# Kernel optimization log

Measured on AMD Instinct MI355X. Metric: run time of the kernel, lower is better.

Reference implementation:

```python
import jax, jax.numpy as jnp
import numpy as np
import math

NUM_HEADS = 16
HEAVY_RATIO = 0.1
RECENT_RATIO = 0.1
ROPE_THETA = 10000.0


def setup_inputs() -> dict:
    key = jax.random.key(0)
    ks = jax.random.split(key, 5)
    b, s, h = 1, 2048, 2048
    return {
        "hidden_states": jax.random.normal(ks[0], (b, s, h), dtype=jnp.float32),
        "Wq": jax.random.normal(ks[1], (h, h), dtype=jnp.float32) * 0.02,
        "Wk": jax.random.normal(ks[2], (h, h), dtype=jnp.float32) * 0.02,
        "Wv": jax.random.normal(ks[3], (h, h), dtype=jnp.float32) * 0.02,
        "Wo": jax.random.normal(ks[4], (h, h), dtype=jnp.float32) * 0.02,
    }


def _rotate_half(x):
    d = x.shape[-1]
    return jnp.concatenate([-x[..., d // 2:], x[..., : d // 2]], axis=-1)


def _rope(q, k, seq_len, head_dim, dtype):
    # LLaMA rotary embedding: inv_freq over even dims, emb = [freqs, freqs]
    inv_freq = 1.0 / (ROPE_THETA ** (jnp.arange(0, head_dim, 2, dtype=jnp.float32) / head_dim))
    pos = jnp.arange(seq_len, dtype=jnp.float32)
    freqs = pos[:, None] * inv_freq[None, :]            # [s, d/2]
    emb = jnp.concatenate([freqs, freqs], axis=-1)       # [s, d]
    cos = jnp.cos(emb).astype(dtype)[None, None]         # [1,1,s,d]
    sin = jnp.sin(emb).astype(dtype)[None, None]
    q = q * cos + _rotate_half(q) * sin
    k = k * cos + _rotate_half(k) * sin
    return q, k


def reference(hidden_states, Wq, Wk, Wv, Wo):
    b, s, hidden = hidden_states.shape
    H = NUM_HEADS
    d = hidden // H

    def proj(W):  # nn.Linear(x) = x @ W.T, then split heads -> [b,H,s,d]
        return (hidden_states @ W.T).reshape(b, s, H, d).transpose(0, 2, 1, 3)

    q, k, v = proj(Wq), proj(Wk), proj(Wv)
    q, k = _rope(q, k, s, d, hidden_states.dtype)

    scores = jnp.einsum("bhqd,bhkd->bhqk", q, k) / math.sqrt(d)  # [b,H,s,s]
    neg = jnp.finfo(scores.dtype).min
    i = jnp.arange(s)[:, None]
    j = jnp.arange(s)[None, :]
    causal = jnp.where(j <= i, jnp.array(0.0, scores.dtype), neg)
    scores = jnp.maximum(scores + causal, neg)

    heavy_budget = int(HEAVY_RATIO * s)
    recent_budget = int(RECENT_RATIO * s)

    # first softmax (fp32), accumulate column importances
    tmp_attn = jax.nn.softmax(scores.astype(jnp.float32), axis=-1).astype(scores.dtype)
    tmp_sum = jnp.sum(tmp_attn, axis=-2)                 # [b,H,s]
    _, topk_idx = jax.lax.top_k(tmp_sum, heavy_budget)   # [b,H,heavy]
    heavy_mask = jnp.any(topk_idx[..., :, None] == jnp.arange(s)[None, None, None, :], axis=-2)  # [b,H,s]

    # recent band: tril(diag=recent) & triu(diag=-recent)  <=>  |i-j| <= recent
    band = jnp.abs(i - j) <= recent_budget               # [s,s]
    mask = heavy_mask[:, :, None, :] | band[None, None]

    scores = jnp.where(mask, scores, neg)
    probs = jax.nn.softmax(scores.astype(jnp.float32), axis=-1).astype(q.dtype)
    attn = jnp.einsum("bhqk,bhkd->bhqd", probs, v)
    attn = attn.transpose(0, 2, 1, 3).reshape(b, s, hidden)
    return attn @ Wo.T
```

## Files before the change

kernel.cpp:

```cpp
#include <hip/hip_runtime.h>
#include <hip/hip_bf16.h>
#include <stdint.h>

#define SEQ   2048
#define HIDN  2048
#define NHEAD 16
#define HDIM  128
#define HEAVY 204
#define RECENT 204

typedef __attribute__((ext_vector_type(4))) float f32x4;
typedef __attribute__((ext_vector_type(8))) short bf16x8;
typedef unsigned short u16;
typedef unsigned int   u32;

static __device__ __forceinline__ u16 f2bf(float f){
  union { float f; u32 u; } v; v.f = f;
  u32 r = (v.u + 0x7FFFu + ((v.u >> 16) & 1u)) >> 16;
  return (u16)r;
}
static __device__ __forceinline__ float bf2f(u16 u){
  union { u32 u; float f; } v; v.u = ((u32)u) << 16;
  return v.f;
}

static __device__ __forceinline__ void gload16(const void* g, void* l){
  __builtin_amdgcn_global_load_lds((const __attribute__((address_space(1))) u32*)g,
                                   (__attribute__((address_space(3))) u32*)l, 16, 0, 0);
}

#define WAITVM(N) asm volatile("s_waitcnt vmcnt(" #N ")" ::: "memory")
#define LGKM0RAW  asm volatile("s_waitcnt lgkmcnt(0)" ::: "memory")
#define BARRAW    __builtin_amdgcn_s_barrier()
#define PRIO1     __builtin_amdgcn_s_setprio(1)
#define PRIO0     __builtin_amdgcn_s_setprio(0)

static __device__ __forceinline__ void stage_tile(const u16* __restrict__ base, size_t stride,
                                                  int row0, u16* __restrict__ lds, int tid){
  const int wbase = tid & ~63;
#pragma unroll
  for (int it = 0; it < 4; ++it){
    int m = it * 256 + tid;
    int row = m >> 4, cp = m & 15;
    gload16(base + (size_t)(row0 + row) * stride + ((cp ^ (row & 7)) * 8),
            lds + (it * 256 + wbase) * 8);
  }
}

static __device__ __forceinline__ void stage64_512(const u16* __restrict__ base, int row0,
                                                   u16* __restrict__ lds, int tid){
#pragma unroll
  for (int it = 0; it < 2; ++it){
    int m = it * 512 + tid;
    int row = m >> 4, cp = m & 15;
    gload16(base + (size_t)(row0 + row) * 2048 + ((cp ^ (row & 7)) * 8),
            lds + (it * 512 + (tid & ~63)) * 8);
  }
}
static __device__ __forceinline__ void stage128_512(const u16* __restrict__ base, int row0,
                                                    u16* __restrict__ lds, int tid){
#pragma unroll
  for (int it = 0; it < 4; ++it){
    int m = it * 512 + tid;
    int row = m >> 4, cp = m & 15;
    gload16(base + (size_t)(row0 + row) * 2048 + ((cp ^ (row & 7)) * 8),
            lds + (it * 512 + (tid & ~63)) * 8);
  }
}

__global__ void k_cvt5(const float* __restrict__ A0, const float* __restrict__ A1,
                       const float* __restrict__ A2, const float* __restrict__ A3,
                       const float* __restrict__ A4, u16* __restrict__ out){
  int id = blockIdx.x * 256 + threadIdx.x;
  int sel = id >> 20, off = (id & 1048575) * 4;
  const float* src = sel == 0 ? A0 : sel == 1 ? A1 : sel == 2 ? A2 : sel == 3 ? A3 : A4;
  float4 v = *(const float4*)(src + off);
  ushort4 o;
  o.x = f2bf(v.x); o.y = f2bf(v.y); o.z = f2bf(v.z); o.w = f2bf(v.w);
  *(ushort4*)(out + (size_t)sel * 4194304 + off) = o;
}

__global__ void k_rope_tab(float* __restrict__ cosT, float* __restrict__ sinT){
  int i = blockIdx.x * 256 + threadIdx.x;
  int pos = i >> 6, j = i & 63;
  float invf = powf(10000.0f, -(float)j * (1.0f / 64.0f));
  float a = (float)pos * invf;
  cosT[i] = cosf(a);
  sinT[i] = sinf(a);
}

__global__ void k_rope2(u16* __restrict__ Qm, u16* __restrict__ Km,
                        const float* __restrict__ cosT, const float* __restrict__ sinT){
  int gid = blockIdx.x * 256 + threadIdx.x;
  u16* M = (gid < 524288) ? Qm : Km;
  int id = gid & 524287;
  int pos = id >> 8, rem = id & 255;
  int h = rem >> 4, j4 = (rem & 15) * 4;
  u16* p = M + (size_t)pos * HIDN + h * HDIM + j4;
  ushort4 lo = *(ushort4*)p;
  ushort4 hi = *(ushort4*)(p + 64);
  float4 c = *(const float4*)(cosT + pos * 64 + j4);
  float4 s = *(const float4*)(sinT + pos * 64 + j4);
  float l0 = bf2f(lo.x), l1 = bf2f(lo.y), l2 = bf2f(lo.z), l3 = bf2f(lo.w);
  float h0 = bf2f(hi.x), h1 = bf2f(hi.y), h2 = bf2f(hi.z), h3 = bf2f(hi.w);
  ushort4 nlo, nhi;
  nlo.x = f2bf(l0 * c.x - h0 * s.x);  nhi.x = f2bf(h0 * c.x + l0 * s.x);
  nlo.y = f2bf(l1 * c.y - h1 * s.y);  nhi.y = f2bf(h1 * c.y + l1 * s.y);
  nlo.z = f2bf(l2 * c.z - h2 * s.z);  nhi.z = f2bf(h2 * c.z + l2 * s.z);
  nlo.w = f2bf(l3 * c.w - h3 * s.w);  nhi.w = f2bf(h3 * c.w + l3 * s.w);
  *(ushort4*)p = nlo;
  *(ushort4*)(p + 64) = nhi;
}

__global__ void k_zero4(float* __restrict__ p, int n4){
  for (int i = blockIdx.x * 256 + threadIdx.x; i < n4; i += gridDim.x * 256)
    ((float4*)p)[i] = (float4){0.f, 0.f, 0.f, 0.f};
}

__global__ __launch_bounds__(512, 1)
void k_g256(const u16* __restrict__ X, const u16* __restrict__ Wq, const u16* __restrict__ Wk,
            const u16* __restrict__ Wv, u16* __restrict__ C0, u16* __restrict__ C1,
            u16* __restrict__ C2){
  __shared__ __align__(16) u16 LA[2][256 * 64];
  __shared__ __align__(16) u16 LB[2][192 * 64];
  const int tid = threadIdx.x;
  const int lane = tid & 63, wvi = tid >> 6;
  const int wm = wvi >> 2, wn = wvi & 3;
  const int g = lane >> 4, c15 = lane & 15;
  const int brow = blockIdx.y * 256;
  const int bcol = blockIdx.x * 192;
  const int NT = 32;

  f32x4 acc[8][3];
#pragma unroll
  for (int m = 0; m < 8; m++)
#pragma unroll
    for (int n = 0; n < 3; n++) acc[m][n] = (f32x4){0.f, 0.f, 0.f, 0.f};

  const int cc0 = ((g ^ (c15 & 7)) * 8);
  bf16x8 af[4][2], bf[3][2];

#define BPTR(rB_) (rB_ < 2048 ? Wq + (size_t)(rB_) * 2048 \
                 : rB_ < 4096 ? Wk + (size_t)((rB_) - 2048) * 2048 \
                              : Wv + (size_t)((rB_) - 4096) * 2048)
#define STGA(grow0, gcol0, ldsb) do { \
  _Pragma("unroll") for (int it = 0; it < 2; ++it){ \
    int m_ = it * 512 + tid; \
    int row_ = m_ >> 3, cp_ = m_ & 7; \
    gload16(X + (size_t)((grow0) + row_) * 2048 + (gcol0) + ((cp_ ^ (row_ & 7)) * 8), \
            (ldsb) + (it * 512 + (tid & ~63)) * 8); \
  } } while(0)
#define STGB128(gcol0, ldsb) do { \
  _Pragma("unroll") for (int it = 0; it < 2; ++it){ \
    int m_ = it * 512 + tid; \
    int row_ = m_ >> 3, cp_ = m_ & 7; \
    int rB_ = bcol + row_; \
    const u16* bp_ = BPTR(rB_); \
    gload16(bp_ + (gcol0) + ((cp_ ^ (row_ & 7)) * 8), \
            (ldsb) + (it * 512 + (tid & ~63)) * 8); \
  } } while(0)
#define STGB64(gcol0, ldsb) do { \
    int row_ = 128 + (tid >> 3), cp_ = tid & 7; \
    int rB_ = bcol + row_; \
    const u16* bp_ = BPTR(rB_); \
    gload16(bp_ + (gcol0) + ((cp_ ^ (row_ & 7)) * 8), \
            (ldsb) + (tid & ~63) * 8); \
  } while(0)
#define RDA(buf, mibase) \
  _Pragma("unroll") for (int mi2 = 0; mi2 < 4; ++mi2){ \
    const u16* pr = &LA[buf][0] + (size_t)(wm * 128 + ((mibase) + mi2) * 16 + c15) * 64; \
    af[mi2][0] = *(const bf16x8*)(pr + cc0); \
    af[mi2][1] = *(const bf16x8*)(pr + (cc0 ^ 32)); \
  }
#define RDB2(buf) \
  _Pragma("unroll") for (int ni2 = 0; ni2 < 2; ++ni2){ \
    const u16* pr = &LB[buf][0] + (size_t)(wn * 48 + ni2 * 16 + c15) * 64; \
    bf[ni2][0] = *(const bf16x8*)(pr + cc0); \
    bf[ni2][1] = *(const bf16x8*)(pr + (cc0 ^ 32)); \
  }
#define RDB1(buf) do { \
    const u16* pr = &LB[buf][0] + (size_t)(wn * 48 + 32 + c15) * 64; \
    bf[2][0] = *(const bf16x8*)(pr + cc0); \
    bf[2][1] = *(const bf16x8*)(pr + (cc0 ^ 32)); \
  } while(0)
#define MM2(mibase) \
  _Pragma("unroll") for (int mi2 = 0; mi2 < 4; ++mi2) \
  _Pragma("unroll") for (int ni2 = 0; ni2 < 2; ++ni2) \
  _Pragma("unroll") for (int kk = 0; kk < 2; ++kk) \
    acc[(mibase) + mi2][ni2] = __builtin_amdgcn_mfma_f32_16x16x32_bf16( \
        af[mi2][kk], bf[ni2][kk], acc[(mibase) + mi2][ni2], 0, 0, 0);
#define MM1(mibase) \
  _Pragma("unroll") for (int mi2 = 0; mi2 < 4; ++mi2) \
  _Pragma("unroll") for (int kk = 0; kk < 2; ++kk) \
    acc[(mibase) + mi2][2] = __builtin_amdgcn_mfma_f32_16x16x32_bf16( \
        af[mi2][kk], bf[2][kk], acc[(mibase) + mi2][2], 0, 0, 0);

  STGA(brow,       0, &LA[0][0]);
  STGA(brow + 128, 0, &LA[0][0] + 128 * 64);
  STGB128(0,  &LB[0][0]);
  STGB64(0,   &LB[0][0] + 128 * 64);
  STGB128(64, &LB[1][0]);
  STGB64(64,  &LB[1][0] + 128 * 64);
  WAITVM(3);
  BARRAW;

  for (int t = 0; t < NT; t += 2){
    const int kn1 = (t + 1) * 64;
    const int kn2 = (t + 2) * 64;
    const int kn3 = (t + 3) * 64;
    RDA(0, 0); RDB2(0);
    STGA(brow, kn1, &LA[1][0]);
    BARRAW; PRIO1; MM2(0); PRIO0; BARRAW;
    RDB1(0);
    STGA(brow + 128, kn1, &LA[1][0] + 128 * 64);
    BARRAW; PRIO1; MM1(0); PRIO0; BARRAW;
    RDA(0, 4);
    if (t + 2 < NT) STGB128(kn2, &LB[0][0]);
    BARRAW; PRIO1; MM1(4); PRIO0; BARRAW;
    if (t + 2 < NT){ STGB64(kn2, &LB[0][0] + 128 * 64); WAITVM(3); }
    else            { WAITVM(0); }
    BARRAW; PRIO1; MM2(4); PRIO0; BARRAW;
    RDA(1, 0); RDB2(1);
    if (t + 2 < NT) STGA(brow, kn2, &LA[0][0]);
    BARRAW; PRIO1; MM2(0); PRIO0; BARRAW;
    RDB1(1);
    if (t + 2 < NT) STGA(brow + 128, kn2, &LA[0][0] + 128 * 64);
    BARRAW; PRIO1; MM1(0); PRIO0; BARRAW;
    RDA(1, 4);
    if (t + 3 < NT) STGB128(kn3, &LB[1][0]);
    BARRAW; PRIO1; MM1(4); PRIO0; BARRAW;
    if (t + 3 < NT){ STGB64(kn3, &LB[1][0] + 128 * 64); WAITVM(3); }
    else if (t + 2 < NT){ WAITVM(0); }
    BARRAW; PRIO1; MM2(4); PRIO0; BARRAW;
  }
#undef BPTR
#undef STGA
#undef STGB128
#undef STGB64
#undef RDA
#undef RDB2
#undef RDB1
#undef MM2
#undef MM1

#pragma unroll
  for (int mi = 0; mi < 8; ++mi)
#pragma unroll
    for (int ni = 0; ni < 3; ++ni){
      int colbase = bcol + wn * 48 + ni * 16;
      int proj = colbase >> 11;
      u16* Cb = proj == 0 ? C0 : proj == 1 ? C1 : C2;
      int lc = (colbase & 2047) + c15;
#pragma unroll
      for (int r = 0; r < 4; ++r){
        int row = brow + wm * 128 + mi * 16 + g * 4 + r;
        Cb[(size_t)row * 2048 + lc] = f2bf(acc[mi][ni][r]);
      }
    }
}

static __device__ __forceinline__ void stage_g(const u16* __restrict__ A, const u16* __restrict__ B,
                                               int brow, int bcol, int k0,
                                               u16* __restrict__ as, u16* __restrict__ bs, int tid){
  const int wbase = tid & ~63;
#pragma unroll
  for (int it = 0; it < 2; ++it){
    int m = it * 256 + tid;
    int row = m >> 2, q = m & 3;
    gload16(A + (size_t)(brow + row) * 2048 + k0 + q * 8, as + (it * 256 + wbase) * 8);
    gload16(B + (size_t)(bcol + row) * 2048 + k0 + q * 8, bs + (it * 256 + wbase) * 8);
  }
}

__global__ __launch_bounds__(256)
void k_gemm_out(const u16* __restrict__ A, const u16* __restrict__ B, float* __restrict__ C){
  __shared__ __align__(16) u16 As[2][128 * 32];
  __shared__ __align__(16) u16 Bs[2][128 * 32];
  const int tid = threadIdx.x;
  const int w = tid >> 6, lane = tid & 63;
  const int wr = w >> 1, wc = w & 1;
  const int g = lane >> 4, c15 = lane & 15;
  const int brow = blockIdx.y * 128, bcol = blockIdx.x * 128;

  f32x4 acc[4][4];
#pragma unroll
  for (int m = 0; m < 4; m++)
#pragma unroll
    for (int n = 0; n < 4; n++) acc[m][n] = (f32x4){0.f, 0.f, 0.f, 0.f};

  stage_g(A, B, brow, bcol, 0, As[0], Bs[0], tid);
  int cur = 0;
  for (int kt = 0; kt < 64; ++kt){
    if (kt + 1 < 64){ stage_g(A, B, brow, bcol, (kt + 1) * 32, As[cur ^ 1], Bs[cur ^ 1], tid);
                      WAITVM(4); }
    else            { WAITVM(0); }
    BARRAW;
    bf16x8 af[4], bfr[4];
#pragma unroll
    for (int m = 0; m < 4; m++) af[m] = *(const bf16x8*)(As[cur] + (wr * 64 + m * 16 + c15) * 32 + g * 8);
#pragma unroll
    for (int n = 0; n < 4; n++) bfr[n] = *(const bf16x8*)(Bs[cur] + (wc * 64 + n * 16 + c15) * 32 + g * 8);
    PRIO1;
#pragma unroll
    for (int m = 0; m < 4; m++)
#pragma unroll
      for (int n = 0; n < 4; n++)
        acc[m][n] = __builtin_amdgcn_mfma_f32_16x16x32_bf16(af[m], bfr[n], acc[m][n], 0, 0, 0);
    PRIO0;
    BARRAW;
    cur ^= 1;
  }
#pragma unroll
  for (int m = 0; m < 4; m++)
#pragma unroll
    for (int n = 0; n < 4; n++)
#pragma unroll
      for (int r = 0; r < 4; r++){
        int row = brow + wr * 64 + m * 16 + g * 4 + r;
        int col = bcol + wc * 64 + n * 16 + c15;
        C[(size_t)row * 2048 + col] = acc[m][n][r];
      }
}

__global__ void k_transpose_v(const u16* __restrict__ V, u16* __restrict__ Vt){
  __shared__ u16 t[32][33];
  int s0 = blockIdx.x * 32, c0 = blockIdx.y * 32;
  int tid = threadIdx.x;
  int r = tid >> 3, cc = (tid & 7) * 4;
  ushort4 v = *(const ushort4*)(V + (size_t)(s0 + r) * 2048 + c0 + cc);
  t[r][cc] = v.x; t[r][cc + 1] = v.y; t[r][cc + 2] = v.z; t[r][cc + 3] = v.w;
  __syncthreads();
  int co = tid >> 3, ro = (tid & 7) * 4;
  ushort4 o;
  o.x = t[ro][co]; o.y = t[ro + 1][co]; o.z = t[ro + 2][co]; o.w = t[ro + 3][co];
  *(ushort4*)(Vt + (size_t)(c0 + co) * 2048 + s0 + ro) = o;
}

__global__ __launch_bounds__(512)
void k_pass1a(const u16* __restrict__ Q, const u16* __restrict__ K, float* __restrict__ rowsum){
  __shared__ __align__(16) u16 Qs[128 * 128];
  __shared__ __align__(16) u16 Ks[2][64 * 128];
  const int tid = threadIdx.x;
  const int wv = tid >> 6, lane = tid & 63;
  const int g = lane >> 4, c15 = lane & 15;
  const int h = blockIdx.y;
  int qb = 0, c = 0;
  { int rem = blockIdx.x; int q = 0;
    while (rem >= ((2 * q + 9) >> 3)){ rem -= (2 * q + 9) >> 3; q++; }
    qb = q; c = rem; }
  const int i0 = qb * 128;
  const int ktend = 2 * qb + 2;
  const int kt0 = c * 8;
  const int kt1 = (ktend < kt0 + 8) ? ktend : (kt0 + 8);
  const u16* Qh = Q + h * HDIM;
  const u16* Kh = K + h * HDIM;
  const float scale = 0.08838834764831845f;
  const int arow = wv * 16 + c15;

  stage128_512(Qh, i0, Qs, tid);
  stage64_512(Kh, kt0 * 64, Ks[0], tid);

  float lsum[4] = {0.f, 0.f, 0.f, 0.f};
  int cur = 0;
  for (int kt = kt0; kt < kt1; ++kt){
    if (kt + 1 < kt1){ stage64_512(Kh, (kt + 1) * 64, Ks[cur ^ 1], tid); WAITVM(2); }
    else             { WAITVM(0); }
    BARRAW;
    const int k0 = kt * 64;
    f32x4 sacc[4];
#pragma unroll
    for (int n = 0; n < 4; n++) sacc[n] = (f32x4){0.f, 0.f, 0.f, 0.f};
#pragma unroll
    for (int ks = 0; ks < 4; ++ks){
      bf16x8 a = *(const bf16x8*)(Qs + arow * 128 + ((ks * 32 + g * 8) ^ ((arow & 7) << 3)));
#pragma unroll
      for (int n = 0; n < 4; n++){
        int brw = n * 16 + c15;
        bf16x8 b = *(const bf16x8*)(Ks[cur] + brw * 128 + ((ks * 32 + g * 8) ^ ((brw & 7) << 3)));
        sacc[n] = __builtin_amdgcn_mfma_f32_16x16x32_bf16(a, b, sacc[n], 0, 0, 0);
      }
    }
    if (kt < 2 * qb){
#pragma unroll
      for (int n = 0; n < 4; n++)
#pragma unroll
        for (int r = 0; r < 4; r++)
          lsum[r] += __expf(sacc[n][r] * scale);
    } else {
#pragma unroll
      for (int n = 0; n < 4; n++){
        int col = k0 + n * 16 + c15;
#pragma unroll
        for (int r = 0; r < 4; r++){
          int rowg = i0 + wv * 16 + g * 4 + r;
          lsum[r] += (col <= rowg) ? __expf(sacc[n][r] * scale) : 0.f;
        }
      }
    }
    BARRAW;
    cur ^= 1;
  }
#pragma unroll
  for (int r = 0; r < 4; r++){
    float v = lsum[r];
    v += __shfl_xor(v, 1); v += __shfl_xor(v, 2);
    v += __shfl_xor(v, 4); v += __shfl_xor(v, 8);
    lsum[r] = v;
  }
  if (c15 == 0){
#pragma unroll
    for (int r = 0; r < 4; r++)
      atomicAdd(&rowsum[h * 2048 + i0 + wv * 16 + g * 4 + r], lsum[r]);
  }
}

__global__ __launch_bounds__(512)
void k_pass1b(const u16* __restrict__ Q, const u16* __restrict__ K,
              const float* __restrict__ rowsum, float* __restrict__ colsum){
  __shared__ __align__(16) u16 Ks[128 * 128];
  __shared__ __align__(16) u16 Qs[2][64 * 128];
  __shared__ float rsb[512];
  const int tid = threadIdx.x;
  const int wv = tid >> 6, lane = tid & 63;
  const int g = lane >> 4, c15 = lane & 15;
  const int h = blockIdx.y;
  int kb = 0, c = 0;
  { int rem = blockIdx.x; int q = 0;
    while (rem >= ((39 - 2 * q) >> 3)){ rem -= (39 - 2 * q) >> 3; q++; }
    kb = q; c = rem; }
  const int k0 = kb * 128;
  const int qt0 = 2 * kb + c * 8;
  const int qt1 = (2 * kb + c * 8 + 8 < 32) ? (2 * kb + c * 8 + 8) : 32;
  const u16* Qh = Q + h * HDIM;
  const u16* Kh = K + h * HDIM;
  const float scale = 0.08838834764831845f;
  const int bcol = wv * 16 + c15;

  { int row = qt0 * 64 + tid;
    float rv = (row < 2048) ? rowsum[h * 2048 + row] : 1.0f;
    rsb[tid] = 1.0f / rv; }
  stage128_512(Kh, k0, Ks, tid);
  stage64_512(Qh, qt0 * 64, Qs[0], tid);
  LGKM0RAW;

  float racc = 0.f;
  int cur = 0;
  for (int qt = qt0; qt < qt1; ++qt){
    if (qt + 1 < qt1){ stage64_512(Qh, (qt + 1) * 64, Qs[cur ^ 1], tid); WAITVM(2); }
    else             { WAITVM(0); }
    BARRAW;
    const int i0q = qt * 64;
    f32x4 sacc[4];
#pragma unroll
    for (int m = 0; m < 4; m++) sacc[m] = (f32x4){0.f, 0.f, 0.f, 0.f};
#pragma unroll
    for (int ks = 0; ks < 4; ++ks){
      bf16x8 b = *(const bf16x8*)(Ks + bcol * 128 + ((ks * 32 + g * 8) ^ ((bcol & 7) << 3)));
#pragma unroll
      for (int m = 0; m < 4; m++){
        int arw = m * 16 + c15;
        bf16x8 a = *(const bf16x8*)(Qs[cur] + arw * 128 + ((ks * 32 + g * 8) ^ ((arw & 7) << 3)));
        sacc[m] = __builtin_amdgcn_mfma_f32_16x16x32_bf16(a, b, sacc[m], 0, 0, 0);
      }
    }
    const int rbase = (qt - qt0) * 64;
    if (qt >= 2 * kb + 2){
#pragma unroll
      for (int m = 0; m < 4; m++)
#pragma unroll
        for (int r = 0; r < 4; r++){
          int rl = m * 16 + g * 4 + r;
          racc += __expf(sacc[m][r] * scale) * rsb[rbase + rl];
        }
    } else {
      const int col = k0 + bcol;
#pragma unroll
      for (int m = 0; m < 4; m++)
#pragma unroll
        for (int r = 0; r < 4; r++){
          int rl = m * 16 + g * 4 + r;
          int rowg = i0q + rl;
          racc += (col <= rowg) ? __expf(sacc[m][r] * scale) * rsb[rbase + rl] : 0.f;
        }
    }
    BARRAW;
    cur ^= 1;
  }
  racc += __shfl_xor(racc, 16);
  racc += __shfl_xor(racc, 32);
  if (g == 0) atomicAdd(&colsum[h * 2048 + k0 + bcol], racc);
}

__global__ __launch_bounds__(1024)
void k_topk(const float* __restrict__ colsum, short* __restrict__ cidx){
  __shared__ float v[2048];
  __shared__ short ix[2048];
  __shared__ short sx[256];
  const int tid = threadIdx.x;
  const int h = blockIdx.x;
  for (int i = tid; i < 2048; i += 1024){ v[i] = colsum[h * 2048 + i]; ix[i] = (short)i; }
  __syncthreads();
  for (int k = 2; k <= 2048; k <<= 1){
    for (int j = k >> 1; j > 0; j >>= 1){
      int i = ((tid / j) * (j << 1)) + (tid % j);
      int l = i + j;
      float vi = v[i], vl = v[l];
      short ii = ix[i], il = ix[l];
      bool before_i = (vi > vl) || (vi == vl && ii < il);
      bool dir = (i & k) == 0;
      if (dir ? !before_i : before_i){ v[i] = vl; v[l] = vi; ix[i] = il; ix[l] = ii; }
      __syncthreads();
    }
  }
  if (tid < 256) sx[tid] = (tid < HEAVY) ? ix[tid] : (short)32767;
  __syncthreads();
  for (int k = 2; k <= 256; k <<= 1){
    for (int j = k >> 1; j > 0; j >>= 1){
      if (tid < 128){
        int i = ((tid / j) * (j << 1)) + (tid % j);
        int l = i + j;
        short a = sx[i], b = sx[l];
        bool asc = (i & k) == 0;
        if (asc ? (a > b) : (a < b)){ sx[i] = b; sx[l] = a; }
      }
      __syncthreads();
    }
  }
  if (tid < 256) cidx[h * 256 + tid] = sx[tid];
}

__global__ void k_gatherK(const u16* __restrict__ Kb, const short* __restrict__ cidx,
                          u16* __restrict__ Kg){
  int gid = blockIdx.x * 256 + threadIdx.x;
  int h = gid >> 12, rem = gid & 4095;
  int slot = rem >> 4, cp = rem & 15;
  int cid = cidx[h * 256 + slot];
  bf16x8 z = (bf16x8){0,0,0,0,0,0,0,0};
  bf16x8 val = (cid < 2048) ? *(const bf16x8*)(Kb + (size_t)cid * 2048 + h * 128 + cp * 8) : z;
  *(bf16x8*)(Kg + ((size_t)h * 256 + slot) * 128 + cp * 8) = val;
}

__global__ void k_gatherV(const u16* __restrict__ Vb, const short* __restrict__ cidx,
                          u16* __restrict__ Vg){
  __shared__ __align__(16) u16 t[32][136];
  int h = blockIdx.x >> 3, s0 = (blockIdx.x & 7) * 32;
  int tid = threadIdx.x;
#pragma unroll
  for (int it = 0; it < 2; ++it){
    int m = it * 256 + tid;
    int s = m >> 4, cp = m & 15;
    int cid = cidx[h * 256 + s0 + s];
    bf16x8 z = (bf16x8){0,0,0,0,0,0,0,0};
    bf16x8 val = (cid < 2048) ? *(const bf16x8*)(Vb + (size_t)cid * 2048 + h * 128 + cp * 8) : z;
    *(bf16x8*)(&t[s][cp * 8]) = val;
  }
  __syncthreads();
#pragma unroll
  for (int i = 0; i < 16; ++i){
    int idx = i * 256 + tid;
    int d = idx >> 5, s = idx & 31;
    Vg[((size_t)h * 128 + d) * 256 + s0 + s] = t[s][d];
  }
}

static __device__ __forceinline__ void load_vf(const u16* __restrict__ Vt,
                                               const u16* __restrict__ Vg,
                                               int h, int e, int g, int c15,
                                               bf16x8 vf[2][8]){
  const bool isg = (e >= 100);
#pragma unroll
  for (int ks2 = 0; ks2 < 2; ++ks2)
#pragma unroll
    for (int f = 0; f < 8; ++f){
      int vrow = f * 16 + c15;
      vf[ks2][f] = isg
        ? *(const bf16x8*)(Vg + ((size_t)h * 128 + vrow) * 256 + (e - 100) * 64 + ks2 * 32 + g * 8)
        : *(const bf16x8*)(Vt + ((size_t)h * 128 + vrow) * 2048 + e * 64 + ks2 * 32 + g * 8);
    }
}

__global__ __launch_bounds__(256)
void k_pass2(const u16* __restrict__ Q, const u16* __restrict__ K, const u16* __restrict__ Vt,
             const u16* __restrict__ Kg, const u16* __restrict__ Vg,
             const short* __restrict__ cidx, u16* __restrict__ attn){
  __shared__ __align__(16) u16 Qs[64 * 128];
  __shared__ __align__(16) u16 Ks[2][64 * 128];
  __shared__ __align__(16) u16 Ps[4][16 * 64];
  __shared__ short cids[256];
  __shared__ int lists[12];
  __shared__ int nact_s;
  const int tid = threadIdx.x;
  const int w = tid >> 6, lane = tid & 63;
  const int g = lane >> 4, c15 = lane & 15;
  const int qb = blockIdx.x, h = blockIdx.y;
  const int i0 = qb * 64;
  const u16* Qh = Q + h * HDIM;
  const u16* Kh = K + h * HDIM;
  const u16* Kgh = Kg + (size_t)h * 256 * 128;
  const float scale = 0.08838834764831845f;
  const int arow = w * 16 + c15;

  if (tid < 256) cids[tid] = cidx[h * 256 + tid];
  __syncthreads();
  if (tid == 0){
    int n = 0;
    int ktb0 = (i0 > RECENT) ? ((i0 - RECENT) >> 6) : 0;
    for (int kt = ktb0; kt <= qb; ++kt) lists[n++] = kt;
    for (int gt = 0; gt < 4; ++gt)
      if ((int)cids[gt * 64] <= i0 - RECENT + 62) lists[n++] = 100 + gt;
    nact_s = n;
  }
  __syncthreads();
  const int nact = nact_s;

  stage_tile(Qh, 2048, i0, Qs, tid);
  { int e = lists[0];
    if (e < 100) stage_tile(Kh, 2048, e * 64, Ks[0], tid);
    else         stage_tile(Kgh, 128, (e - 100) * 64, Ks[0], tid); }
  bf16x8 vf[2][8];
  load_vf(Vt, Vg, h, lists[0], g, c15, vf);
  WAITVM(16);
  BARRAW;

  f32x4 oacc[8];
#pragma unroll
  for (int f = 0; f < 8; f++) oacc[f] = (f32x4){0.f, 0.f, 0.f, 0.f};
  float lsum[4] = {0.f, 0.f, 0.f, 0.f};

  int cur = 0;
  for (int i = 0; i < nact; ++i){
    const int e = lists[i];
    const bool isg = (e >= 100);
    const bool nxt = (i + 1 < nact);
    if (nxt){
      int e2 = lists[i + 1];
      if (e2 < 100) stage_tile(Kh, 2048, e2 * 64, Ks[cur ^ 1], tid);
      else          stage_tile(Kgh, 128, (e2 - 100) * 64, Ks[cur ^ 1], tid);
      WAITVM(20);
    } else {
      WAITVM(16);
    }
    BARRAW;
    f32x4 sacc[4];
#pragma unroll
    for (int n = 0; n < 4; n++) sacc[n] = (f32x4){0.f, 0.f, 0.f, 0.f};
#pragma unroll
    for (int ks = 0; ks < 4; ++ks){
      bf16x8 a = *(const bf16x8*)(Qs + arow * 128 + ((ks * 32 + g * 8) ^ ((arow & 7) << 3)));
#pragma unroll
      for (int n = 0; n < 4; n++){
        int brw = n * 16 + c15;
        bf16x8 b = *(const bf16x8*)(Ks[cur] + brw * 128 + ((ks * 32 + g * 8) ^ ((brw & 7) << 3)));
        sacc[n] = __builtin_amdgcn_mfma_f32_16x16x32_bf16(a, b, sacc[n], 0, 0, 0);
      }
    }
#pragma unroll
    for (int n = 0; n < 4; n++){
      int cid = isg ? (int)cids[(e - 100) * 64 + n * 16 + c15] : (e * 64 + n * 16 + c15);
#pragma unroll
      for (int r = 0; r < 4; r++){
        int rowg = i0 + w * 16 + g * 4 + r;
        int dist = rowg - cid;
        bool valid = (cid <= rowg) && (isg ? (dist > RECENT) : (dist <= RECENT));
        float ev = valid ? __expf(sacc[n][r] * scale) : 0.f;
        lsum[r] += ev;
        int prow = g * 4 + r;
        Ps[w][prow * 64 + ((n * 16 + c15) ^ ((prow & 7) << 3))] = f2bf(ev);
      }
    }
    if (nxt) WAITVM(4); else WAITVM(0);
    PRIO1;
#pragma unroll
    for (int ks2 = 0; ks2 < 2; ++ks2){
      bf16x8 pa = *(const bf16x8*)(&Ps[w][c15 * 64 + ((ks2 * 32 + g * 8) ^ ((c15 & 7) << 3))]);
#pragma unroll
      for (int f = 0; f < 8; ++f)
        oacc[f] = __builtin_amdgcn_mfma_f32_16x16x32_bf16(pa, vf[ks2][f], oacc[f], 0, 0, 0);
    }
    PRIO0;
    if (nxt) load_vf(Vt, Vg, h, lists[i + 1], g, c15, vf);
    BARRAW;
    cur ^= 1;
  }
  float rinv[4];
#pragma unroll
  for (int r = 0; r < 4; r++){
    float v = lsum[r];
    v += __shfl_xor(v, 1); v += __shfl_xor(v, 2);
    v += __shfl_xor(v, 4); v += __shfl_xor(v, 8);
    rinv[r] = 1.0f / v;
  }
#pragma unroll
  for (int f = 0; f < 8; f++)
#pragma unroll
    for (int r = 0; r < 4; r++){
      int rowg = i0 + w * 16 + g * 4 + r;
      attn[(size_t)rowg * 2048 + h * HDIM + f * 16 + c15] = f2bf(oacc[f][r] * rinv[r]);
    }
}

extern "C" void kernel_launch(void* const* d_in, const int* in_sizes, int n_in,
                              void* d_out, int out_size, void* d_ws, size_t ws_size,
                              hipStream_t stream){
  const float* X  = (const float*)d_in[0];
  const float* Wq = (const float*)d_in[1];
  const float* Wk = (const float*)d_in[2];
  const float* Wv = (const float*)d_in[3];
  const float* Wo = (const float*)d_in[4];

  char* w = (char*)d_ws;
  const size_t MB8 = (size_t)2048 * 2048 * 2;
  u16* Xb  = (u16*)(w);
  u16* Wqb = (u16*)(w + 1 * MB8);
  u16* Wkb = (u16*)(w + 2 * MB8);
  u16* Wvb = (u16*)(w + 3 * MB8);
  u16* Wob = (u16*)(w + 4 * MB8);
  u16* Qb  = (u16*)(w + 5 * MB8);
  u16* Kb  = (u16*)(w + 6 * MB8);
  u16* Vb  = (u16*)(w + 7 * MB8);
  u16* Vtb   = Wqb;
  u16* attnb = Xb;
  char* p = w + 8 * MB8;
  float* cosT = (float*)p;              p += 524288;
  float* sinT = (float*)p;              p += 524288;
  float* colsum = (float*)p;            p += 131072;
  float* rowsum = (float*)p;            p += 131072;
  short* cidx  = (short*)p;             p += 16 * 256 * 2;
  u16*   Kg    = (u16*)p;               p += (size_t)16 * 256 * 128 * 2;
  u16*   Vg    = (u16*)p;

  dim3 b256(256);

  k_cvt5<<<20480, b256, 0, stream>>>(X, Wq, Wk, Wv, Wo, Xb);
  k_rope_tab<<<512, b256, 0, stream>>>(cosT, sinT);
  k_zero4<<<64, b256, 0, stream>>>(colsum, 65536 / 4);

  k_g256<<<dim3(32, 8), dim3(512), 0, stream>>>(Xb, Wqb, Wkb, Wvb, Qb, Kb, Vb);
  k_rope2<<<4096, b256, 0, stream>>>(Qb, Kb, cosT, sinT);
  k_transpose_v<<<dim3(64, 64), b256, 0, stream>>>(Vb, Vtb);

  k_pass1a<<<dim3(40, 16), dim3(512), 0, stream>>>(Qb, Kb, rowsum);
  k_pass1b<<<dim3(40, 16), dim3(512), 0, stream>>>(Qb, Kb, rowsum, colsum);
  k_topk<<<16, dim3(1024), 0, stream>>>(colsum, cidx);
  k_gatherK<<<256, b256, 0, stream>>>(Kb, cidx, Kg);
  k_gatherV<<<128, b256, 0, stream>>>(Vb, cidx, Vg);
  k_pass2<<<dim3(32, 16), b256, 0, stream>>>(Qb, Kb, Vtb, Kg, Vg, cidx, attnb);

  k_gemm_out<<<dim3(16, 16), b256, 0, stream>>>(attnb, Wob, (float*)d_out);
}
```

Before: 278.9 us.

## Merge small launches into combined kernels and restructure pass1 to register-resident tiles

Several small kernels are merged into combined launches selected by block index: the convert, rope-table and zero kernels become one, rope and V transpose become one, and the K and V gathers become one. This is meant to cut per-launch overhead and tail gaps between dependent launches. Separately, pass1a and pass1b drop to 256 threads with each wave owning 32 rows. The stationary Q or K operand now sits in registers instead of LDS, which cuts LDS use and reads but raises register pressure.

```diff
diff --git a/kernel.cpp b/kernel.cpp
--- a/kernel.cpp
+++ b/kernel.cpp
@@ -30,7 +30,6 @@
 }
 
 #define WAITVM(N) asm volatile("s_waitcnt vmcnt(" #N ")" ::: "memory")
-#define LGKM0RAW  asm volatile("s_waitcnt lgkmcnt(0)" ::: "memory")
 #define BARRAW    __builtin_amdgcn_s_barrier()
 #define PRIO1     __builtin_amdgcn_s_setprio(1)
 #define PRIO0     __builtin_amdgcn_s_setprio(0)
@@ -47,74 +46,70 @@
   }
 }
 
-static __device__ __forceinline__ void stage64_512(const u16* __restrict__ base, int row0,
-                                                   u16* __restrict__ lds, int tid){
-#pragma unroll
-  for (int it = 0; it < 2; ++it){
-    int m = it * 512 + tid;
-    int row = m >> 4, cp = m & 15;
-    gload16(base + (size_t)(row0 + row) * 2048 + ((cp ^ (row & 7)) * 8),
-            lds + (it * 512 + (tid & ~63)) * 8);
-  }
-}
-static __device__ __forceinline__ void stage128_512(const u16* __restrict__ base, int row0,
-                                                    u16* __restrict__ lds, int tid){
-#pragma unroll
-  for (int it = 0; it < 4; ++it){
-    int m = it * 512 + tid;
-    int row = m >> 4, cp = m & 15;
-    gload16(base + (size_t)(row0 + row) * 2048 + ((cp ^ (row & 7)) * 8),
-            lds + (it * 512 + (tid & ~63)) * 8);
-  }
-}
-
-__global__ void k_cvt5(const float* __restrict__ A0, const float* __restrict__ A1,
+__global__ void k_prep(const float* __restrict__ A0, const float* __restrict__ A1,
                        const float* __restrict__ A2, const float* __restrict__ A3,
-                       const float* __restrict__ A4, u16* __restrict__ out){
-  int id = blockIdx.x * 256 + threadIdx.x;
-  int sel = id >> 20, off = (id & 1048575) * 4;
-  const float* src = sel == 0 ? A0 : sel == 1 ? A1 : sel == 2 ? A2 : sel == 3 ? A3 : A4;
-  float4 v = *(const float4*)(src + off);
-  ushort4 o;
-  o.x = f2bf(v.x); o.y = f2bf(v.y); o.z = f2bf(v.z); o.w = f2bf(v.w);
-  *(ushort4*)(out + (size_t)sel * 4194304 + off) = o;
-}
-
-__global__ void k_rope_tab(float* __restrict__ cosT, float* __restrict__ sinT){
-  int i = blockIdx.x * 256 + threadIdx.x;
-  int pos = i >> 6, j = i & 63;
-  float invf = powf(10000.0f, -(float)j * (1.0f / 64.0f));
-  float a = (float)pos * invf;
-  cosT[i] = cosf(a);
-  sinT[i] = sinf(a);
-}
-
-__global__ void k_rope2(u16* __restrict__ Qm, u16* __restrict__ Km,
-                        const float* __restrict__ cosT, const float* __restrict__ sinT){
-  int gid = blockIdx.x * 256 + threadIdx.x;
-  u16* M = (gid < 524288) ? Qm : Km;
-  int id = gid & 524287;
-  int pos = id >> 8, rem = id & 255;
-  int h = rem >> 4, j4 = (rem & 15) * 4;
-  u16* p = M + (size_t)pos * HIDN + h * HDIM + j4;
-  ushort4 lo = *(ushort4*)p;
-  ushort4 hi = *(ushort4*)(p + 64);
-  float4 c = *(const float4*)(cosT + pos * 64 + j4);
-  float4 s = *(const float4*)(sinT + pos * 64 + j4);
-  float l0 = bf2f(lo.x), l1 = bf2f(lo.y), l2 = bf2f(lo.z), l3 = bf2f(lo.w);
-  float h0 = bf2f(hi.x), h1 = bf2f(hi.y), h2 = bf2f(hi.z), h3 = bf2f(hi.w);
-  ushort4 nlo, nhi;
-  nlo.x = f2bf(l0 * c.x - h0 * s.x);  nhi.x = f2bf(h0 * c.x + l0 * s.x);
-  nlo.y = f2bf(l1 * c.y - h1 * s.y);  nhi.y = f2bf(h1 * c.y + l1 * s.y);
-  nlo.z = f2bf(l2 * c.z - h2 * s.z);  nhi.z = f2bf(h2 * c.z + l2 * s.z);
-  nlo.w = f2bf(l3 * c.w - h3 * s.w);  nhi.w = f2bf(h3 * c.w + l3 * s.w);
-  *(ushort4*)p = nlo;
-  *(ushort4*)(p + 64) = nhi;
-}
-
-__global__ void k_zero4(float* __restrict__ p, int n4){
-  for (int i = blockIdx.x * 256 + threadIdx.x; i < n4; i += gridDim.x * 256)
-    ((float4*)p)[i] = (float4){0.f, 0.f, 0.f, 0.f};
+                       const float* __restrict__ A4, u16* __restrict__ out,
+                       float* __restrict__ cosT, float* __restrict__ sinT,
+                       float* __restrict__ colsum){
+  int b = blockIdx.x, tid = threadIdx.x;
+  if (b < 20480){
+    int id = b * 256 + tid;
+    int sel = id >> 20, off = (id & 1048575) * 4;
+    const float* src = sel == 0 ? A0 : sel == 1 ? A1 : sel == 2 ? A2 : sel == 3 ? A3 : A4;
+    float4 v = *(const float4*)(src + off);
+    ushort4 o;
+    o.x = f2bf(v.x); o.y = f2bf(v.y); o.z = f2bf(v.z); o.w = f2bf(v.w);
+    *(ushort4*)(out + (size_t)sel * 4194304 + off) = o;
+  } else if (b < 20992){
+    int i = (b - 20480) * 256 + tid;
+    int pos = i >> 6, j = i & 63;
+    float invf = powf(10000.0f, -(float)j * (1.0f / 64.0f));
+    float a = (float)pos * invf;
+    cosT[i] = cosf(a);
+    sinT[i] = sinf(a);
+  } else {
+    int i = (b - 20992) * 256 + tid;
+    if (i < 16384) ((float4*)colsum)[i] = (float4){0.f, 0.f, 0.f, 0.f};
+  }
+}
+
+__global__ void k_post(u16* __restrict__ Qm, u16* __restrict__ Km,
+                       const float* __restrict__ cosT, const float* __restrict__ sinT,
+                       const u16* __restrict__ V, u16* __restrict__ Vt){
+  __shared__ u16 t[32][33];
+  int b = blockIdx.x, tid = threadIdx.x;
+  if (b < 4096){
+    int gid = b * 256 + tid;
+    u16* M = (gid < 524288) ? Qm : Km;
+    int id = gid & 524287;
+    int pos = id >> 8, rem = id & 255;
+    int h = rem >> 4, j4 = (rem & 15) * 4;
+    u16* p = M + (size_t)pos * HIDN + h * HDIM + j4;
+    ushort4 lo = *(ushort4*)p;
+    ushort4 hi = *(ushort4*)(p + 64);
+    float4 c = *(const float4*)(cosT + pos * 64 + j4);
+    float4 s = *(const float4*)(sinT + pos * 64 + j4);
+    float l0 = bf2f(lo.x), l1 = bf2f(lo.y), l2 = bf2f(lo.z), l3 = bf2f(lo.w);
+    float h0 = bf2f(hi.x), h1 = bf2f(hi.y), h2 = bf2f(hi.z), h3 = bf2f(hi.w);
+    ushort4 nlo, nhi;
+    nlo.x = f2bf(l0 * c.x - h0 * s.x);  nhi.x = f2bf(h0 * c.x + l0 * s.x);
+    nlo.y = f2bf(l1 * c.y - h1 * s.y);  nhi.y = f2bf(h1 * c.y + l1 * s.y);
+    nlo.z = f2bf(l2 * c.z - h2 * s.z);  nhi.z = f2bf(h2 * c.z + l2 * s.z);
+    nlo.w = f2bf(l3 * c.w - h3 * s.w);  nhi.w = f2bf(h3 * c.w + l3 * s.w);
+    *(ushort4*)p = nlo;
+    *(ushort4*)(p + 64) = nhi;
+  } else {
+    int b2 = b - 4096;
+    int s0 = (b2 & 63) * 32, c0 = (b2 >> 6) * 32;
+    int r = tid >> 3, cc = (tid & 7) * 4;
+    ushort4 v = *(const ushort4*)(V + (size_t)(s0 + r) * 2048 + c0 + cc);
+    t[r][cc] = v.x; t[r][cc + 1] = v.y; t[r][cc + 2] = v.z; t[r][cc + 3] = v.w;
+    __syncthreads();
+    int co = tid >> 3, ro = (tid & 7) * 4;
+    ushort4 o;
+    o.x = t[ro][co]; o.y = t[ro + 1][co]; o.z = t[ro + 2][co]; o.w = t[ro + 3][co];
+    *(ushort4*)(Vt + (size_t)(c0 + co) * 2048 + s0 + ro) = o;
+  }
 }
 
 __global__ __launch_bounds__(512, 1)
@@ -322,23 +317,8 @@
       }
 }
 
-__global__ void k_transpose_v(const u16* __restrict__ V, u16* __restrict__ Vt){
-  __shared__ u16 t[32][33];
-  int s0 = blockIdx.x * 32, c0 = blockIdx.y * 32;
-  int tid = threadIdx.x;
-  int r = tid >> 3, cc = (tid & 7) * 4;
-  ushort4 v = *(const ushort4*)(V + (size_t)(s0 + r) * 2048 + c0 + cc);
-  t[r][cc] = v.x; t[r][cc + 1] = v.y; t[r][cc + 2] = v.z; t[r][cc + 3] = v.w;
-  __syncthreads();
-  int co = tid >> 3, ro = (tid & 7) * 4;
-  ushort4 o;
-  o.x = t[ro][co]; o.y = t[ro + 1][co]; o.z = t[ro + 2][co]; o.w = t[ro + 3][co];
-  *(ushort4*)(Vt + (size_t)(c0 + co) * 2048 + s0 + ro) = o;
-}
-
-__global__ __launch_bounds__(512)
+__global__ __launch_bounds__(256)
 void k_pass1a(const u16* __restrict__ Q, const u16* __restrict__ K, float* __restrict__ rowsum){
-  __shared__ __align__(16) u16 Qs[128 * 128];
   __shared__ __align__(16) u16 Ks[2][64 * 128];
   const int tid = threadIdx.x;
   const int wv = tid >> 6, lane = tid & 63;
@@ -355,71 +335,80 @@
   const u16* Qh = Q + h * HDIM;
   const u16* Kh = K + h * HDIM;
   const float scale = 0.08838834764831845f;
-  const int arow = wv * 16 + c15;
-
-  stage128_512(Qh, i0, Qs, tid);
-  stage64_512(Kh, kt0 * 64, Ks[0], tid);
-
-  float lsum[4] = {0.f, 0.f, 0.f, 0.f};
+  const int wb = wv * 32;
+
+  bf16x8 qfr[2][4];
+#pragma unroll
+  for (int m = 0; m < 2; m++)
+#pragma unroll
+    for (int ks = 0; ks < 4; ks++)
+      qfr[m][ks] = *(const bf16x8*)(Qh + (size_t)(i0 + wb + m * 16 + c15) * 2048 + ks * 32 + g * 8);
+
+  stage_tile(Kh, 2048, kt0 * 64, Ks[0], tid);
+
+  float rs[2][4] = {{0.f,0.f,0.f,0.f},{0.f,0.f,0.f,0.f}};
   int cur = 0;
   for (int kt = kt0; kt < kt1; ++kt){
-    if (kt + 1 < kt1){ stage64_512(Kh, (kt + 1) * 64, Ks[cur ^ 1], tid); WAITVM(2); }
+    if (kt + 1 < kt1){ stage_tile(Kh, 2048, (kt + 1) * 64, Ks[cur ^ 1], tid); WAITVM(4); }
     else             { WAITVM(0); }
     BARRAW;
     const int k0 = kt * 64;
-    f32x4 sacc[4];
-#pragma unroll
-    for (int n = 0; n < 4; n++) sacc[n] = (f32x4){0.f, 0.f, 0.f, 0.f};
+    f32x4 sacc[2][4];
+#pragma unroll
+    for (int m = 0; m < 2; m++)
+#pragma unroll
+      for (int n = 0; n < 4; n++) sacc[m][n] = (f32x4){0.f, 0.f, 0.f, 0.f};
 #pragma unroll
     for (int ks = 0; ks < 4; ++ks){
-      bf16x8 a = *(const bf16x8*)(Qs + arow * 128 + ((ks * 32 + g * 8) ^ ((arow & 7) << 3)));
 #pragma unroll
       for (int n = 0; n < 4; n++){
         int brw = n * 16 + c15;
         bf16x8 b = *(const bf16x8*)(Ks[cur] + brw * 128 + ((ks * 32 + g * 8) ^ ((brw & 7) << 3)));
-        sacc[n] = __builtin_amdgcn_mfma_f32_16x16x32_bf16(a, b, sacc[n], 0, 0, 0);
+#pragma unroll
+        for (int m = 0; m < 2; m++)
+          sacc[m][n] = __builtin_amdgcn_mfma_f32_16x16x32_bf16(qfr[m][ks], b, sacc[m][n], 0, 0, 0);
       }
     }
     if (kt < 2 * qb){
 #pragma unroll
-      for (int n = 0; n < 4; n++)
-#pragma unroll
-        for (int r = 0; r < 4; r++)
-          lsum[r] += __expf(sacc[n][r] * scale);
+      for (int m = 0; m < 2; m++)
+#pragma unroll
+        for (int n = 0; n < 4; n++)
+#pragma unroll
+          for (int r = 0; r < 4; r++)
+            rs[m][r] += __expf(sacc[m][n][r] * scale);
     } else {
 #pragma unroll
       for (int n = 0; n < 4; n++){
         int col = k0 + n * 16 + c15;
 #pragma unroll
-        for (int r = 0; r < 4; r++){
-          int rowg = i0 + wv * 16 + g * 4 + r;
-          lsum[r] += (col <= rowg) ? __expf(sacc[n][r] * scale) : 0.f;
-        }
+        for (int m = 0; m < 2; m++)
+#pragma unroll
+          for (int r = 0; r < 4; r++){
+            int rowg = i0 + wb + m * 16 + g * 4 + r;
+            rs[m][r] += (col <= rowg) ? __expf(sacc[m][n][r] * scale) : 0.f;
+          }
       }
     }
     BARRAW;
     cur ^= 1;
   }
 #pragma unroll
-  for (int r = 0; r < 4; r++){
-    float v = lsum[r];
-    v += __shfl_xor(v, 1); v += __shfl_xor(v, 2);
-    v += __shfl_xor(v, 4); v += __shfl_xor(v, 8);
-    lsum[r] = v;
-  }
-  if (c15 == 0){
-#pragma unroll
-    for (int r = 0; r < 4; r++)
-      atomicAdd(&rowsum[h * 2048 + i0 + wv * 16 + g * 4 + r], lsum[r]);
-  }
-}
-
-__global__ __launch_bounds__(512)
+  for (int m = 0; m < 2; m++)
+#pragma unroll
+    for (int r = 0; r < 4; r++){
+      float v = rs[m][r];
+      v += __shfl_xor(v, 1); v += __shfl_xor(v, 2);
+      v += __shfl_xor(v, 4); v += __shfl_xor(v, 8);
+      if (c15 == 0)
+        atomicAdd(&rowsum[h * 2048 + i0 + wb + m * 16 + g * 4 + r], v);
+    }
+}
+
+__global__ __launch_bounds__(256)
 void k_pass1b(const u16* __restrict__ Q, const u16* __restrict__ K,
               const float* __restrict__ rowsum, float* __restrict__ colsum){
-  __shared__ __align__(16) u16 Ks[128 * 128];
   __shared__ __align__(16) u16 Qs[2][64 * 128];
-  __shared__ float rsb[512];
   const int tid = threadIdx.x;
   const int wv = tid >> 6, lane = tid & 63;
   const int g = lane >> 4, c15 = lane & 15;
@@ -434,61 +423,79 @@
   const u16* Qh = Q + h * HDIM;
   const u16* Kh = K + h * HDIM;
   const float scale = 0.08838834764831845f;
-  const int bcol = wv * 16 + c15;
-
-  { int row = qt0 * 64 + tid;
-    float rv = (row < 2048) ? rowsum[h * 2048 + row] : 1.0f;
-    rsb[tid] = 1.0f / rv; }
-  stage128_512(Kh, k0, Ks, tid);
-  stage64_512(Qh, qt0 * 64, Qs[0], tid);
-  LGKM0RAW;
-
-  float racc = 0.f;
+  const int wb = wv * 32;
+  const float* rsrow = rowsum + h * 2048;
+
+  bf16x8 kfr[2][4];
+#pragma unroll
+  for (int m = 0; m < 2; m++)
+#pragma unroll
+    for (int ks = 0; ks < 4; ks++)
+      kfr[m][ks] = *(const bf16x8*)(Kh + (size_t)(k0 + wb + m * 16 + c15) * 2048 + ks * 32 + g * 8);
+
+  stage_tile(Qh, 2048, qt0 * 64, Qs[0], tid);
+
+  float racc[2][4] = {{0.f,0.f,0.f,0.f},{0.f,0.f,0.f,0.f}};
   int cur = 0;
   for (int qt = qt0; qt < qt1; ++qt){
-    if (qt + 1 < qt1){ stage64_512(Qh, (qt + 1) * 64, Qs[cur ^ 1], tid); WAITVM(2); }
+    if (qt + 1 < qt1){ stage_tile(Qh, 2048, (qt + 1) * 64, Qs[cur ^ 1], tid); WAITVM(4); }
     else             { WAITVM(0); }
     BARRAW;
     const int i0q = qt * 64;
-    f32x4 sacc[4];
-#pragma unroll
-    for (int m = 0; m < 4; m++) sacc[m] = (f32x4){0.f, 0.f, 0.f, 0.f};
+    float rw[4];
+#pragma unroll
+    for (int n = 0; n < 4; n++)
+      rw[n] = 1.0f / rsrow[i0q + n * 16 + c15];
+    f32x4 sacc[2][4];
+#pragma unroll
+    for (int m = 0; m < 2; m++)
+#pragma unroll
+      for (int n = 0; n < 4; n++) sacc[m][n] = (f32x4){0.f, 0.f, 0.f, 0.f};
 #pragma unroll
     for (int ks = 0; ks < 4; ++ks){
-      bf16x8 b = *(const bf16x8*)(Ks + bcol * 128 + ((ks * 32 + g * 8) ^ ((bcol & 7) << 3)));
-#pragma unroll
-      for (int m = 0; m < 4; m++){
-        int arw = m * 16 + c15;
-        bf16x8 a = *(const bf16x8*)(Qs[cur] + arw * 128 + ((ks * 32 + g * 8) ^ ((arw & 7) << 3)));
-        sacc[m] = __builtin_amdgcn_mfma_f32_16x16x32_bf16(a, b, sacc[m], 0, 0, 0);
-      }
-    }
-    const int rbase = (qt - qt0) * 64;
+#pragma unroll
+      for (int n = 0; n < 4; n++){
+        int brw = n * 16 + c15;
+        bf16x8 b = *(const bf16x8*)(Qs[cur] + brw * 128 + ((ks * 32 + g * 8) ^ ((brw & 7) << 3)));
+#pragma unroll
+        for (int m = 0; m < 2; m++)
+          sacc[m][n] = __builtin_amdgcn_mfma_f32_16x16x32_bf16(kfr[m][ks], b, sacc[m][n], 0, 0, 0);
+      }
+    }
     if (qt >= 2 * kb + 2){
 #pragma unroll
-      for (int m = 0; m < 4; m++)
-#pragma unroll
-        for (int r = 0; r < 4; r++){
-          int rl = m * 16 + g * 4 + r;
-          racc += __expf(sacc[m][r] * scale) * rsb[rbase + rl];
-        }
+      for (int m = 0; m < 2; m++)
+#pragma unroll
+        for (int n = 0; n < 4; n++)
+#pragma unroll
+          for (int r = 0; r < 4; r++)
+            racc[m][r] += __expf(sacc[m][n][r] * scale) * rw[n];
     } else {
-      const int col = k0 + bcol;
-#pragma unroll
-      for (int m = 0; m < 4; m++)
-#pragma unroll
-        for (int r = 0; r < 4; r++){
-          int rl = m * 16 + g * 4 + r;
-          int rowg = i0q + rl;
-          racc += (col <= rowg) ? __expf(sacc[m][r] * scale) * rsb[rbase + rl] : 0.f;
-        }
+#pragma unroll
+      for (int n = 0; n < 4; n++){
+        int colq = i0q + n * 16 + c15;
+#pragma unroll
+        for (int m = 0; m < 2; m++)
+#pragma unroll
+          for (int r = 0; r < 4; r++){
+            int rowk = k0 + wb + m * 16 + g * 4 + r;
+            racc[m][r] += (rowk <= colq) ? __expf(sacc[m][n][r] * scale) * rw[n] : 0.f;
+          }
+      }
     }
     BARRAW;
     cur ^= 1;
   }
-  racc += __shfl_xor(racc, 16);
-  racc += __shfl_xor(racc, 32);
-  if (g == 0) atomicAdd(&colsum[h * 2048 + k0 + bcol], racc);
+#pragma unroll
+  for (int m = 0; m < 2; m++)
+#pragma unroll
+    for (int r = 0; r < 4; r++){
+      float v = racc[m][r];
+      v += __shfl_xor(v, 1); v += __shfl_xor(v, 2);
+      v += __shfl_xor(v, 4); v += __shfl_xor(v, 8);
+      if (c15 == 0)
+        atomicAdd(&colsum[h * 2048 + k0 + wb + m * 16 + g * 4 + r], v);
+    }
 }
 
 __global__ __launch_bounds__(1024)
@@ -529,37 +536,38 @@
   if (tid < 256) cidx[h * 256 + tid] = sx[tid];
 }
 
-__global__ void k_gatherK(const u16* __restrict__ Kb, const short* __restrict__ cidx,
-                          u16* __restrict__ Kg){
-  int gid = blockIdx.x * 256 + threadIdx.x;
-  int h = gid >> 12, rem = gid & 4095;
-  int slot = rem >> 4, cp = rem & 15;
-  int cid = cidx[h * 256 + slot];
-  bf16x8 z = (bf16x8){0,0,0,0,0,0,0,0};
-  bf16x8 val = (cid < 2048) ? *(const bf16x8*)(Kb + (size_t)cid * 2048 + h * 128 + cp * 8) : z;
-  *(bf16x8*)(Kg + ((size_t)h * 256 + slot) * 128 + cp * 8) = val;
-}
-
-__global__ void k_gatherV(const u16* __restrict__ Vb, const short* __restrict__ cidx,
-                          u16* __restrict__ Vg){
+__global__ void k_gatherKV(const u16* __restrict__ Kb, const u16* __restrict__ Vb,
+                           const short* __restrict__ cidx,
+                           u16* __restrict__ Kg, u16* __restrict__ Vg){
   __shared__ __align__(16) u16 t[32][136];
-  int h = blockIdx.x >> 3, s0 = (blockIdx.x & 7) * 32;
-  int tid = threadIdx.x;
-#pragma unroll
-  for (int it = 0; it < 2; ++it){
-    int m = it * 256 + tid;
-    int s = m >> 4, cp = m & 15;
-    int cid = cidx[h * 256 + s0 + s];
+  int b = blockIdx.x, tid = threadIdx.x;
+  if (b < 256){
+    int gid = b * 256 + tid;
+    int h = gid >> 12, rem = gid & 4095;
+    int slot = rem >> 4, cp = rem & 15;
+    int cid = cidx[h * 256 + slot];
     bf16x8 z = (bf16x8){0,0,0,0,0,0,0,0};
-    bf16x8 val = (cid < 2048) ? *(const bf16x8*)(Vb + (size_t)cid * 2048 + h * 128 + cp * 8) : z;
-    *(bf16x8*)(&t[s][cp * 8]) = val;
-  }
-  __syncthreads();
-#pragma unroll
-  for (int i = 0; i < 16; ++i){
-    int idx = i * 256 + tid;
-    int d = idx >> 5, s = idx & 31;
-    Vg[((size_t)h * 128 + d) * 256 + s0 + s] = t[s][d];
+    bf16x8 val = (cid < 2048) ? *(const bf16x8*)(Kb + (size_t)cid * 2048 + h * 128 + cp * 8) : z;
+    *(bf16x8*)(Kg + ((size_t)h * 256 + slot) * 128 + cp * 8) = val;
+  } else {
+    int b2 = b - 256;
+    int h = b2 >> 3, s0 = (b2 & 7) * 32;
+#pragma unroll
+    for (int it = 0; it < 2; ++it){
+      int m = it * 256 + tid;
+      int s = m >> 4, cp = m & 15;
+      int cid = cidx[h * 256 + s0 + s];
+      bf16x8 z = (bf16x8){0,0,0,0,0,0,0,0};
+      bf16x8 val = (cid < 2048) ? *(const bf16x8*)(Vb + (size_t)cid * 2048 + h * 128 + cp * 8) : z;
+      *(bf16x8*)(&t[s][cp * 8]) = val;
+    }
+    __syncthreads();
+#pragma unroll
+    for (int i = 0; i < 16; ++i){
+      int idx = i * 256 + tid;
+      int d = idx >> 5, s = idx & 31;
+      Vg[((size_t)h * 128 + d) * 256 + s0 + s] = t[s][d];
+    }
   }
 }
 
@@ -731,19 +739,15 @@
 
   dim3 b256(256);
 
-  k_cvt5<<<20480, b256, 0, stream>>>(X, Wq, Wk, Wv, Wo, Xb);
-  k_rope_tab<<<512, b256, 0, stream>>>(cosT, sinT);
-  k_zero4<<<64, b256, 0, stream>>>(colsum, 65536 / 4);
+  k_prep<<<21056, b256, 0, stream>>>(X, Wq, Wk, Wv, Wo, Xb, cosT, sinT, colsum);
 
   k_g256<<<dim3(32, 8), dim3(512), 0, stream>>>(Xb, Wqb, Wkb, Wvb, Qb, Kb, Vb);
-  k_rope2<<<4096, b256, 0, stream>>>(Qb, Kb, cosT, sinT);
-  k_transpose_v<<<dim3(64, 64), b256, 0, stream>>>(Vb, Vtb);
-
-  k_pass1a<<<dim3(40, 16), dim3(512), 0, stream>>>(Qb, Kb, rowsum);
-  k_pass1b<<<dim3(40, 16), dim3(512), 0, stream>>>(Qb, Kb, rowsum, colsum);
+  k_post<<<8192, b256, 0, stream>>>(Qb, Kb, cosT, sinT, Vb, Vtb);
+
+  k_pass1a<<<dim3(40, 16), b256, 0, stream>>>(Qb, Kb, rowsum);
+  k_pass1b<<<dim3(40, 16), b256, 0, stream>>>(Qb, Kb, rowsum, colsum);
   k_topk<<<16, dim3(1024), 0, stream>>>(colsum, cidx);
-  k_gatherK<<<256, b256, 0, stream>>>(Kb, cidx, Kg);
-  k_gatherV<<<128, b256, 0, stream>>>(Vb, cidx, Vg);
+  k_gatherKV<<<384, b256, 0, stream>>>(Kb, Vb, cidx, Kg, Vg);
   k_pass2<<<dim3(32, 16), b256, 0, stream>>>(Qb, Kb, Vtb, Kg, Vg, cidx, attnb);
 
   k_gemm_out<<<dim3(16, 16), b256, 0, stream>>>(attnb, Wob, (float*)d_out);
```

Result: faster. 262.4 us (-5.9%).
